# Optimization experiments

Measured on AMD Instinct MI355X. Metric: run time of the kernel, lower is better.

Reference implementation:

```python
import jax, jax.numpy as jnp
import numpy as np

N_NODES = 50000
N_EDGES = 400000
C_IN = 256
HID = 512
C_OUT = 128
N_GRAPHS = 64
BN_EPS = 1e-5


def setup_inputs() -> dict:
    key = jax.random.key(0)
    ks = jax.random.split(key, 18)
    s_in = 1.0 / np.sqrt(C_IN)
    s_h = 1.0 / np.sqrt(HID)
    inp = {
        'x': jax.random.normal(ks[0], (N_NODES, C_IN), jnp.float32),
        'edge_index': jax.random.randint(ks[1], (2, N_EDGES), 0, N_NODES, jnp.int32).astype(jnp.int64),
        'batch': jnp.sort(jax.random.randint(ks[2], (N_NODES,), 0, N_GRAPHS, jnp.int32)).astype(jnp.int64),
        'enc_w': jax.random.normal(ks[3], (C_IN, HID), jnp.float32) * s_in,
        'enc_b': jax.random.normal(ks[4], (HID,), jnp.float32) * s_in,
        'conv_w0': jax.random.normal(ks[5], (2, HID, HID), jnp.float32) * s_h,
        'conv_b0': jax.random.normal(ks[6], (2, HID), jnp.float32) * s_h,
        'bn0_g': jax.random.uniform(ks[7], (2, HID), jnp.float32, 0.5, 1.5),
        'bn0_b': jax.random.normal(ks[8], (2, HID), jnp.float32) * 0.1,
        'conv_w1': jax.random.normal(ks[9], (2, HID, HID), jnp.float32) * s_h,
        'conv_b1': jax.random.normal(ks[10], (2, HID), jnp.float32) * s_h,
        'bn1_g': jax.random.uniform(ks[11], (2, HID), jnp.float32, 0.5, 1.5),
        'bn1_b': jax.random.normal(ks[12], (2, HID), jnp.float32) * 0.1,
        'lin_w': jax.random.normal(ks[13], (HID, HID), jnp.float32) * s_h,
        'lin_b': jax.random.normal(ks[14], (HID,), jnp.float32) * s_h,
        'clf_w': jax.random.normal(ks[15], (HID, C_OUT), jnp.float32) * s_h,
        'clf_b': jax.random.normal(ks[16], (C_OUT,), jnp.float32) * s_h,
    }
    return inp


def _bn_eval(h, gamma, beta):
    # BatchNorm1d in eval mode with default buffers: running_mean=0, running_var=1
    return h * (gamma / jnp.sqrt(1.0 + BN_EPS)) + beta


def reference(x, edge_index, batch, enc_w, enc_b, conv_w0, conv_b0, bn0_g, bn0_b,
              conv_w1, conv_b1, bn1_g, bn1_b, lin_w, lin_b, clf_w, clf_b):
    src, dst = edge_index[0], edge_index[1]
    n = x.shape[0]
    # encoder (gbn output is dead code in the original forward; omitted)
    x = x @ enc_w + enc_b  # [N, HID]
    # GIN_Net: 2 GINConv layers, eps=0, sum aggregation, MLP = Lin-BN-ReLU-Lin-BN
    for i in range(2):
        agg = jax.ops.segment_sum(x[src], dst, num_segments=n)  # scatter-add of neighbor feats
        h = x + agg  # (1 + eps) * x + aggr, eps = 0
        h = h @ conv_w0[i] + conv_b0[i]
        h = jax.nn.relu(_bn_eval(h, bn0_g[i], bn0_b[i]))
        h = h @ conv_w1[i] + conv_b1[i]
        h = _bn_eval(h, bn1_g[i], bn1_b[i])
        # inter-layer relu (dropout p=0 / eval -> identity); skipped after last layer
        x = h if i == 1 else jax.nn.relu(h)
    # global mean pooling over graphs
    sums = jax.ops.segment_sum(x, batch, num_segments=N_GRAPHS)  # [G, HID]
    counts = jax.ops.segment_sum(jnp.ones((n,), x.dtype), batch, num_segments=N_GRAPHS)
    pooled = sums / jnp.maximum(counts, 1.0)[:, None]
    g = jax.nn.gelu(pooled @ lin_w + lin_b, approximate=False)
    # dropout(0.5) identity in eval mode
    return g @ clf_w + clf_b  # [G, C_OUT]
```

## Files before the change

### kernel.cpp

```cpp
#include <hip/hip_runtime.h>
#include <hip/hip_bf16.h>
#include <stdint.h>

#define NN 50000
#define M_PAD 50048
#define NE 400000
#define CIN 256
#define KF 320
#define HID 512
#define COUT 128
#define NG 64
#define SCAN_NB ((NN + 255) / 256)
#define MT128 (M_PAD / 128)
#define GEMM_BLOCKS 512

typedef short bf16x8 __attribute__((ext_vector_type(8)));
typedef float f32x4 __attribute__((ext_vector_type(4)));
typedef unsigned int u32x2 __attribute__((ext_vector_type(2)));

__device__ inline float bf2f(unsigned short u) {
    union { unsigned int i; float f; } v; v.i = ((unsigned int)u) << 16; return v.f;
}
__device__ inline unsigned short f2bf(float f) {
    union { float f; unsigned int u; } v; v.f = f;
    unsigned int r = v.u + 0x7fffu + ((v.u >> 16) & 1u);
    return (unsigned short)(r >> 16);
}

__device__ inline void async16(const void* g, void* l) {
    __builtin_amdgcn_global_load_lds((const __attribute__((address_space(1))) void*)g,
                                     (__attribute__((address_space(3))) void*)l, 16, 0, 0);
}


__global__ void k_f32_to_bf16(const float* __restrict__ in, unsigned short* __restrict__ out, int n4) {
    int i = blockIdx.x * blockDim.x + threadIdx.x;
    if (i < n4) {
        float4 v = ((const float4*)in)[i];
        ushort4 o;
        o.x = f2bf(v.x); o.y = f2bf(v.y); o.z = f2bf(v.z); o.w = f2bf(v.w);
        ((ushort4*)out)[i] = o;
    }
}

__global__ void k_transpose_cvt(const float* __restrict__ in, unsigned short* __restrict__ out, int K, int N) {
    __shared__ float tile[32][33];
    int bx = blockIdx.x * 32, by = blockIdx.y * 32;
    int tx = threadIdx.x & 31, ty = threadIdx.x >> 5;
    for (int i = 0; i < 32; i += 8)
        tile[ty + i][tx] = in[(size_t)(by + ty + i) * N + bx + tx];
    __syncthreads();
    for (int i = 0; i < 32; i += 8)
        out[(size_t)(bx + ty + i) * K + by + tx] = f2bf(tile[tx][ty + i]);
}

__global__ void k_fuse_w0(const float* __restrict__ enc_w, const float* __restrict__ enc_b,
                          const float* __restrict__ W0, unsigned short* __restrict__ WfT) {
    int n = blockIdx.x;
    __shared__ float col[HID];
    for (int j = threadIdx.x; j < HID; j += 256) col[j] = W0[(size_t)j * HID + n];
    __syncthreads();
    int k = threadIdx.x;
    float acc = 0.f;
    for (int j = 0; j < HID; j++) acc += enc_w[(size_t)k * HID + j] * col[j];
    WfT[(size_t)n * KF + k] = f2bf(acc);
    if (k == 0) {
        float v = 0.f;
        for (int j = 0; j < HID; j++) v += enc_b[j] * col[j];
        WfT[(size_t)n * KF + 256] = f2bf(v);
    }
    if (k >= 1 && k < 64) WfT[(size_t)n * KF + 256 + k] = 0;
}

__global__ void k_affine(const float* __restrict__ enc_b,
                         const float* __restrict__ cb0, const float* __restrict__ bg0, const float* __restrict__ bb0,
                         const float* __restrict__ cb1, const float* __restrict__ bg1, const float* __restrict__ bb1,
                         float* __restrict__ scale, float* __restrict__ shift) {
    int c = threadIdx.x;
    const float inv = 0.9999950000374997f;
    scale[c] = 1.f; shift[c] = enc_b[c];
    for (int l = 0; l < 2; l++) {
        float s0 = bg0[l * HID + c] * inv;
        scale[(1 + 2 * l) * HID + c] = s0;
        shift[(1 + 2 * l) * HID + c] = cb0[l * HID + c] * s0 + bb0[l * HID + c];
        float s1 = bg1[l * HID + c] * inv;
        scale[(2 + 2 * l) * HID + c] = s1;
        shift[(2 + 2 * l) * HID + c] = cb1[l * HID + c] * s1 + bb1[l * HID + c];
    }
}


__global__ void k_hist(const int* __restrict__ dst, int* __restrict__ indeg, int n) {
    int i = blockIdx.x * blockDim.x + threadIdx.x;
    if (i < n) atomicAdd(&indeg[dst[i]], 1);
}

__global__ void k_scan1(const int* __restrict__ indeg, int* __restrict__ local,
                        int* __restrict__ blocksum, int n) {
    __shared__ int s[256];
    int t = threadIdx.x;
    int i = blockIdx.x * 256 + t;
    int v = (i < n) ? indeg[i] : 0;
    s[t] = v;
    __syncthreads();
    for (int d = 1; d < 256; d <<= 1) {
        int u = (t >= d) ? s[t - d] : 0;
        __syncthreads();
        s[t] += u;
        __syncthreads();
    }
    if (i < n) local[i] = s[t] - v;
    if (t == 255) blocksum[blockIdx.x] = s[255];
}

__global__ void k_scan2(int* __restrict__ blocksum, int nb) {
    __shared__ int s[256];
    int t = threadIdx.x;
    int v = (t < nb) ? blocksum[t] : 0;
    s[t] = v;
    __syncthreads();
    for (int d = 1; d < 256; d <<= 1) {
        int u = (t >= d) ? s[t - d] : 0;
        __syncthreads();
        s[t] += u;
        __syncthreads();
    }
    if (t < nb) blocksum[t] = s[t] - v;
}

__global__ void k_scan3(const int* __restrict__ local, const int* __restrict__ blocksum,
                        const int* __restrict__ indeg, int* __restrict__ off,
                        int* __restrict__ cursor, int n) {
    int i = blockIdx.x * 256 + threadIdx.x;
    if (i < n) {
        int o = local[i] + blocksum[blockIdx.x];
        off[i] = o;
        cursor[i] = o;
        if (i == n - 1) off[n] = o + indeg[i];
    }
}

__global__ void k_fill(const int* __restrict__ src, const int* __restrict__ dst,
                       int* __restrict__ cursor, int* __restrict__ csr, int n) {
    int i = blockIdx.x * blockDim.x + threadIdx.x;
    if (i < n) {
        int p = atomicAdd(&cursor[dst[i]], 1);
        csr[p] = src[i];
    }
}


__global__ void k_aggregate0(const unsigned short* __restrict__ x, const int* __restrict__ off,
                             const int* __restrict__ csr, unsigned short* __restrict__ z) {
    int wid = (int)((blockIdx.x * blockDim.x + threadIdx.x) >> 6);
    if (wid >= NN) return;
    int lane = threadIdx.x & 63;
    const uint2* xr = (const uint2*)x;
    uint2 v = xr[(size_t)wid * 64 + lane];
    float acc[4];
    {
        unsigned short* p = (unsigned short*)&v;
        for (int i = 0; i < 4; i++) acc[i] = bf2f(p[i]);
    }
    int e0 = off[wid], e1 = off[wid + 1];
    int e = e0;
    for (; e + 3 < e1; e += 4) {
        int u0 = csr[e], u1 = csr[e + 1], u2 = csr[e + 2], u3 = csr[e + 3];
        uint2 v0 = xr[(size_t)u0 * 64 + lane];
        uint2 v1 = xr[(size_t)u1 * 64 + lane];
        uint2 v2 = xr[(size_t)u2 * 64 + lane];
        uint2 v3 = xr[(size_t)u3 * 64 + lane];
        unsigned short* p0 = (unsigned short*)&v0;
        unsigned short* p1 = (unsigned short*)&v1;
        unsigned short* p2 = (unsigned short*)&v2;
        unsigned short* p3 = (unsigned short*)&v3;
#pragma unroll
        for (int i = 0; i < 4; i++)
            acc[i] += (bf2f(p0[i]) + bf2f(p1[i])) + (bf2f(p2[i]) + bf2f(p3[i]));
    }
    for (; e < e1; e++) {
        int u = csr[e];
        uint2 vu = xr[(size_t)u * 64 + lane];
        unsigned short* p = (unsigned short*)&vu;
#pragma unroll
        for (int i = 0; i < 4; i++) acc[i] += bf2f(p[i]);
    }
    uint2 o;
    unsigned short* po = (unsigned short*)&o;
    for (int i = 0; i < 4; i++) po[i] = f2bf(acc[i]);
    uint2* zr = (uint2*)z;
    zr[(size_t)wid * 80 + lane] = o;
    if (lane < 16) {
        uint2 ex; ex.x = 0; ex.y = 0;
        if (lane == 0) ex.x = (unsigned)f2bf((float)(1 + e1 - e0));
        zr[(size_t)wid * 80 + 64 + lane] = ex;
    }
}


__global__ void k_aggregate(const unsigned short* __restrict__ x, const int* __restrict__ off,
                            const int* __restrict__ csr, unsigned short* __restrict__ h) {
    int wid = (int)((blockIdx.x * blockDim.x + threadIdx.x) >> 6);
    if (wid >= NN) return;
    int lane = threadIdx.x & 63;
    const uint4* xr = (const uint4*)x;
    uint4 v = xr[(size_t)wid * 64 + lane];
    float acc[8];
    {
        unsigned short* p = (unsigned short*)&v;
        for (int i = 0; i < 8; i++) acc[i] = bf2f(p[i]);
    }
    int e0 = off[wid], e1 = off[wid + 1];
    int e = e0;
    for (; e + 3 < e1; e += 4) {
        int u0 = csr[e], u1 = csr[e + 1], u2 = csr[e + 2], u3 = csr[e + 3];
        uint4 v0 = xr[(size_t)u0 * 64 + lane];
        uint4 v1 = xr[(size_t)u1 * 64 + lane];
        uint4 v2 = xr[(size_t)u2 * 64 + lane];
        uint4 v3 = xr[(size_t)u3 * 64 + lane];
        unsigned short* p0 = (unsigned short*)&v0;
        unsigned short* p1 = (unsigned short*)&v1;
        unsigned short* p2 = (unsigned short*)&v2;
        unsigned short* p3 = (unsigned short*)&v3;
#pragma unroll
        for (int i = 0; i < 8; i++)
            acc[i] += (bf2f(p0[i]) + bf2f(p1[i])) + (bf2f(p2[i]) + bf2f(p3[i]));
    }
    for (; e < e1; e++) {
        int u = csr[e];
        uint4 vu = xr[(size_t)u * 64 + lane];
        unsigned short* p = (unsigned short*)&vu;
#pragma unroll
        for (int i = 0; i < 8; i++) acc[i] += bf2f(p[i]);
    }
    uint4 o;
    unsigned short* po = (unsigned short*)&o;
    for (int i = 0; i < 8; i++) po[i] = f2bf(acc[i]);
    ((uint4*)h)[(size_t)wid * 64 + lane] = o;
}


template <int RELU, int NSTEPS>
__global__ __launch_bounds__(256, 2) void k_gemm(const unsigned short* __restrict__ A,
                                                 const unsigned short* __restrict__ WT,
                                                 const float* __restrict__ scale,
                                                 const float* __restrict__ shift,
                                                 unsigned short* __restrict__ out) {
    constexpr int K = NSTEPS * 64;
    __shared__ char lds[69632];
    const int tid = threadIdx.x, w = tid >> 6, lane = tid & 63;
    const int wr = w >> 1, wc = w & 1;
    const int lr = lane & 15, lh = lane >> 4;

    {
        float2 s2 = *(const float2*)(scale + tid * 2);
        float2 h2 = *(const float2*)(shift + tid * 2);
        *(float2*)(lds + 65536 + tid * 8) = s2;
        *(float2*)(lds + 67584 + tid * 8) = h2;
    }
    __syncthreads();

    const int b = blockIdx.x;
    const int xcd = b & 7, slot = b >> 3;
    const int xs = (xcd < 4) ? xcd * 196 : 784 + (xcd - 4) * 195;
    const int xcnt = (xcd < 4) ? 196 : 195;
    const int ntiles = (xcnt - slot + 63) >> 6;
    int t = xs + slot;

    int ldsoff[4], roff[4];
#pragma unroll
    for (int ci = 0; ci < 4; ci++) {
        int cc = w * 4 + ci;
        ldsoff[ci] = cc * 1024;
        roff[ci] = ((cc >> 1) * 16 + lr) * K + (cc & 1) * 32 + lh * 8;
    }

    const unsigned short* gA[4];
    const unsigned short* gB[4];
    {
        int tile_m = (t >> 2) * 128, n0 = (t & 3) * 128;
#pragma unroll
        for (int ci = 0; ci < 4; ci++) {
            gA[ci] = A + (size_t)tile_m * K + roff[ci];
            gB[ci] = WT + (size_t)n0 * K + roff[ci];
        }
    }

#pragma unroll
    for (int ci = 0; ci < 4; ci++) { async16(gA[ci], lds + ldsoff[ci]); async16(gB[ci], lds + 16384 + ldsoff[ci]); }
#pragma unroll
    for (int ci = 0; ci < 4; ci++) { async16(gA[ci] + 64, lds + 32768 + ldsoff[ci]); async16(gB[ci] + 64, lds + 32768 + 16384 + ldsoff[ci]); }

    for (int i = 0; i < ntiles; i++) {
        const bool last = (i == ntiles - 1);
        const unsigned short* nA[4];
        const unsigned short* nB[4];
        {
            int tn = last ? t : t + 64;
            int tile_m = (tn >> 2) * 128, n0 = (tn & 3) * 128;
#pragma unroll
            for (int ci = 0; ci < 4; ci++) {
                nA[ci] = A + (size_t)tile_m * K + roff[ci];
                nB[ci] = WT + (size_t)n0 * K + roff[ci];
            }
        }

        f32x4 acc[4][4];
#pragma unroll
        for (int x = 0; x < 4; x++)
#pragma unroll
            for (int y = 0; y < 4; y++) acc[x][y] = f32x4{0.f, 0.f, 0.f, 0.f};

#pragma unroll
        for (int ks = 0; ks < NSTEPS; ks++) {
            const int cur = (ks & 1) << 15;
            if (i > 0 && ks < 2)                 asm volatile("s_waitcnt vmcnt(24)" ::: "memory");
            else if (last && ks == NSTEPS - 1)   asm volatile("s_waitcnt vmcnt(0)" ::: "memory");
            else                                 asm volatile("s_waitcnt vmcnt(8)" ::: "memory");
            __builtin_amdgcn_s_barrier();
            __builtin_amdgcn_sched_barrier(0);
#pragma unroll
            for (int kf = 0; kf < 2; kf++) {
                bf16x8 a[4], bb[4];
#pragma unroll
                for (int mf = 0; mf < 4; mf++)
                    a[mf] = *(const bf16x8*)(lds + cur + ((wr * 4 + mf) * 2 + kf) * 1024 + lane * 16);
#pragma unroll
                for (int nf = 0; nf < 4; nf++)
                    bb[nf] = *(const bf16x8*)(lds + cur + 16384 + ((wc * 4 + nf) * 2 + kf) * 1024 + lane * 16);
#pragma unroll
                for (int mf = 0; mf < 4; mf++)
#pragma unroll
                    for (int nf = 0; nf < 4; nf++)
                        acc[mf][nf] = __builtin_amdgcn_mfma_f32_16x16x32_bf16(bb[nf], a[mf], acc[mf][nf], 0, 0, 0);
            }
            __builtin_amdgcn_sched_barrier(0);
            __builtin_amdgcn_s_barrier();
            if (ks + 2 < NSTEPS) {
                int ko = (ks + 2) << 6;
#pragma unroll
                for (int ci = 0; ci < 4; ci++) {
                    async16(gA[ci] + ko, lds + cur + ldsoff[ci]);
                    async16(gB[ci] + ko, lds + cur + 16384 + ldsoff[ci]);
                }
            } else if (!last) {
                int ko = (ks + 2 - NSTEPS) << 6;
#pragma unroll
                for (int ci = 0; ci < 4; ci++) {
                    async16(nA[ci] + ko, lds + cur + ldsoff[ci]);
                    async16(nB[ci] + ko, lds + cur + 16384 + ldsoff[ci]);
                }
            }
        }

        {
            int tile_m = (t >> 2) * 128, n0 = (t & 3) * 128;
#pragma unroll
            for (int nf = 0; nf < 4; nf++) {
                int col = n0 + wc * 64 + nf * 16 + lh * 4;
                f32x4 sc = *(const f32x4*)(lds + 65536 + ((wc * 64 + nf * 16 + lh * 4) << 2) + (n0 << 2));
                f32x4 sh = *(const f32x4*)(lds + 67584 + ((wc * 64 + nf * 16 + lh * 4) << 2) + (n0 << 2));
#pragma unroll
                for (int mf = 0; mf < 4; mf++) {
                    int row = tile_m + wr * 64 + mf * 16 + lr;
                    float y0 = acc[mf][nf][0] * sc[0] + sh[0];
                    float y1 = acc[mf][nf][1] * sc[1] + sh[1];
                    float y2 = acc[mf][nf][2] * sc[2] + sh[2];
                    float y3 = acc[mf][nf][3] * sc[3] + sh[3];
                    if (RELU) {
                        y0 = fmaxf(y0, 0.f); y1 = fmaxf(y1, 0.f);
                        y2 = fmaxf(y2, 0.f); y3 = fmaxf(y3, 0.f);
                    }
                    u32x2 pd;
                    pd[0] = (unsigned)f2bf(y0) | ((unsigned)f2bf(y1) << 16);
                    pd[1] = (unsigned)f2bf(y2) | ((unsigned)f2bf(y3) << 16);
                    unsigned long long ap = (unsigned long long)(out + (size_t)row * HID + col);
                    asm volatile("global_store_dwordx2 %0, %1, off" :: "v"(ap), "v"(pd) : "memory");
                }
            }
        }

        if (!last) {
#pragma unroll
            for (int ci = 0; ci < 4; ci++) { gA[ci] = nA[ci]; gB[ci] = nB[ci]; }
            t += 64;
        }
    }
}


__global__ void k_bounds(const int* __restrict__ batch, int* __restrict__ bounds) {
    int t = threadIdx.x;
    if (t <= NG) {
        int lo = 0, hi = NN;
        while (lo < hi) { int mid = (lo + hi) >> 1; if (batch[mid] < t) lo = mid + 1; else hi = mid; }
        bounds[t] = lo;
    }
}

__global__ void k_pool(const unsigned short* __restrict__ x, const int* __restrict__ bounds,
                       float* __restrict__ pooled) {
    int g = blockIdx.x, s = blockIdx.y, t = threadIdx.x;
    int b0 = bounds[g], b1 = bounds[g + 1];
    int len = b1 - b0;
    int r0 = b0 + (int)((long long)len * s / 8);
    int r1 = b0 + (int)((long long)len * (s + 1) / 8);
    float acc = 0.f;
    for (int r = r0; r < r1; r++) acc += bf2f(x[(size_t)r * HID + t]);
    if (r1 > r0) atomicAdd(&pooled[g * HID + t], acc);
}

__global__ void k_tailgemm(const float* __restrict__ pooledSum, const int* __restrict__ bounds,
                           const float* __restrict__ W1, const float* __restrict__ scale,
                           const float* __restrict__ shift, float* __restrict__ xfp) {
    int g = blockIdx.x, t = threadIdx.x;
    __shared__ float row[HID];
    int cnt = bounds[g + 1] - bounds[g];
    float invc = 1.f / fmaxf((float)cnt, 1.f);
    row[t] = pooledSum[g * HID + t] * invc;
    __syncthreads();
    float acc = 0.f;
    for (int k = 0; k < HID; k++) acc += row[k] * W1[(size_t)k * HID + t];
    xfp[g * HID + t] = acc * scale[t] + shift[t];
}

__global__ void k_head1(const float* __restrict__ xfp, const float* __restrict__ lin_w,
                        const float* __restrict__ lin_b, float* __restrict__ gout) {
    int g = blockIdx.x, t = threadIdx.x;
    __shared__ float row[HID];
    row[t] = xfp[g * HID + t];
    __syncthreads();
    float acc = lin_b[t];
    for (int k = 0; k < HID; k++) acc += row[k] * lin_w[(size_t)k * HID + t];
    gout[g * HID + t] = 0.5f * acc * (1.f + erff(acc * 0.7071067811865475f));
}

__global__ void k_head2(const float* __restrict__ gbuf, const float* __restrict__ clf_w,
                        const float* __restrict__ clf_b, float* __restrict__ out) {
    int g = blockIdx.x, t = threadIdx.x;
    __shared__ float row[HID];
    for (int k = t; k < HID; k += 128) row[k] = gbuf[g * HID + k];
    __syncthreads();
    float acc = clf_b[t];
    for (int k = 0; k < HID; k++) acc += row[k] * clf_w[(size_t)k * COUT + t];
    out[g * COUT + t] = acc;
}


extern "C" void kernel_launch(void* const* d_in, const int* in_sizes, int n_in,
                              void* d_out, int out_size, void* d_ws, size_t ws_size,
                              hipStream_t stream) {
    const float* x_f32   = (const float*)d_in[0];
    const int*   ei      = (const int*)d_in[1];
    const int*   batch   = (const int*)d_in[2];
    const float* enc_w   = (const float*)d_in[3];
    const float* enc_b   = (const float*)d_in[4];
    const float* conv_w0 = (const float*)d_in[5];
    const float* conv_b0 = (const float*)d_in[6];
    const float* bn0_g   = (const float*)d_in[7];
    const float* bn0_b   = (const float*)d_in[8];
    const float* conv_w1 = (const float*)d_in[9];
    const float* conv_b1 = (const float*)d_in[10];
    const float* bn1_g   = (const float*)d_in[11];
    const float* bn1_b   = (const float*)d_in[12];
    const float* lin_w   = (const float*)d_in[13];
    const float* lin_b   = (const float*)d_in[14];
    const float* clf_w   = (const float*)d_in[15];
    const float* clf_b   = (const float*)d_in[16];
    const int* srcp = ei;
    const int* dstp = ei + NE;

    char* ws = (char*)d_ws;
    size_t o = 0;
    auto alloc = [&](size_t b) { size_t r = o; o += (b + 255) & ~(size_t)255; return r; };
    unsigned short* buf0 = (unsigned short*)(ws + alloc((size_t)M_PAD * HID * 2));
    unsigned short* buf1 = (unsigned short*)(ws + alloc((size_t)M_PAD * HID * 2));
    unsigned short* buf2 = (unsigned short*)(ws + alloc((size_t)M_PAD * HID * 2));
    unsigned short* xbf  = buf0;
    unsigned short* zbuf = buf2;
    unsigned short* WfT  = (unsigned short*)(ws + alloc((size_t)HID * KF * 2));
    unsigned short* c0T  = (unsigned short*)(ws + alloc((size_t)HID * HID * 2));
    unsigned short* c1T  = (unsigned short*)(ws + alloc((size_t)HID * HID * 2));
    float* aff_scale = (float*)(ws + alloc(5 * HID * 4));
    float* aff_shift = (float*)(ws + alloc(5 * HID * 4));
    int* indeg  = (int*)(ws + alloc((size_t)NN * 4));
    int* off    = (int*)(ws + alloc((size_t)(NN + 1) * 4));
    int* cursor = (int*)(ws + alloc((size_t)NN * 4));
    int* csr    = (int*)(ws + alloc((size_t)NE * 4));
    int* scan_local = (int*)(ws + alloc((size_t)NN * 4));
    int* scan_bsum  = (int*)(ws + alloc((size_t)256 * 4));
    int* bounds = (int*)(ws + alloc((size_t)(NG + 1) * 4));
    float* pooledSum = (float*)(ws + alloc((size_t)NG * HID * 4));
    float* xfp       = (float*)(ws + alloc((size_t)NG * HID * 4));
    float* gbuf      = (float*)(ws + alloc((size_t)NG * HID * 4));
    (void)ws_size; (void)n_in; (void)in_sizes; (void)out_size;

    hipMemsetAsync(indeg, 0, (size_t)NN * 4, stream);
    hipMemsetAsync(pooledSum, 0, (size_t)NG * HID * 4, stream);

    k_f32_to_bf16<<<(NN * CIN / 4 + 255) / 256, 256, 0, stream>>>(x_f32, xbf, NN * CIN / 4);
    k_fuse_w0<<<HID, 256, 0, stream>>>(enc_w, enc_b, conv_w0, WfT);
    k_transpose_cvt<<<dim3(16, 16), 256, 0, stream>>>(conv_w0 + HID * HID, c0T, HID, HID);
    k_transpose_cvt<<<dim3(16, 16), 256, 0, stream>>>(conv_w1, c1T, HID, HID);
    k_affine<<<1, 512, 0, stream>>>(enc_b, conv_b0, bn0_g, bn0_b, conv_b1, bn1_g, bn1_b,
                                    aff_scale, aff_shift);

    k_hist<<<(NE + 255) / 256, 256, 0, stream>>>(dstp, indeg, NE);
    k_scan1<<<SCAN_NB, 256, 0, stream>>>(indeg, scan_local, scan_bsum, NN);
    k_scan2<<<1, 256, 0, stream>>>(scan_bsum, SCAN_NB);
    k_scan3<<<SCAN_NB, 256, 0, stream>>>(scan_local, scan_bsum, indeg, off, cursor, NN);
    k_fill<<<(NE + 255) / 256, 256, 0, stream>>>(srcp, dstp, cursor, csr, NE);
    k_bounds<<<1, 128, 0, stream>>>(batch, bounds);

    k_aggregate0<<<(NN * 64) / 256, 256, 0, stream>>>(xbf, off, csr, zbuf);
    k_gemm<1, KF / 64><<<GEMM_BLOCKS, 256, 0, stream>>>(zbuf, WfT,
                                                        aff_scale + 1 * HID, aff_shift + 1 * HID, buf0);
    k_gemm<1, HID / 64><<<GEMM_BLOCKS, 256, 0, stream>>>(buf0, c1T,
                                                         aff_scale + 2 * HID, aff_shift + 2 * HID, buf2);

    k_aggregate<<<(NN * 64) / 256, 256, 0, stream>>>(buf2, off, csr, buf1);
    k_gemm<1, HID / 64><<<GEMM_BLOCKS, 256, 0, stream>>>(buf1, c0T,
                                                         aff_scale + 3 * HID, aff_shift + 3 * HID, buf2);

    k_pool<<<dim3(NG, 8), 512, 0, stream>>>(buf2, bounds, pooledSum);
    k_tailgemm<<<NG, 512, 0, stream>>>(pooledSum, bounds, conv_w1 + HID * HID,
                                       aff_scale + 4 * HID, aff_shift + 4 * HID, xfp);
    k_head1<<<NG, 512, 0, stream>>>(xfp, lin_w, lin_b, gbuf);
    k_head2<<<NG, 128, 0, stream>>>(gbuf, clf_w, clf_b, (float*)d_out);
}
```

Baseline: 478.9 us.

## Triple-buffer A tiles and keep per-column scale/shift in registers

The GEMM pipeline now gives the A operand three LDS stages and B two, so A loads are issued three k-steps ahead while B stays two ahead. Each block's column tile is fixed across its persistent loop, which allows scale/shift to be held in registers instead of LDS and the next-tile pointers to be advanced by a constant stride. Raises s_setprio around the MFMA section. The LDS footprint grows to 80KB, which may limit two blocks per CU, and the vmcnt bookkeeping becomes more fragile.

```diff
diff --git a/kernel.cpp b/kernel.cpp
--- a/kernel.cpp
+++ b/kernel.cpp
@@ -247,18 +247,10 @@
                                                  const float* __restrict__ shift,
                                                  unsigned short* __restrict__ out) {
     constexpr int K = NSTEPS * 64;
-    __shared__ char lds[69632];
+    __shared__ char lds[81920];
     const int tid = threadIdx.x, w = tid >> 6, lane = tid & 63;
     const int wr = w >> 1, wc = w & 1;
     const int lr = lane & 15, lh = lane >> 4;
-
-    {
-        float2 s2 = *(const float2*)(scale + tid * 2);
-        float2 h2 = *(const float2*)(shift + tid * 2);
-        *(float2*)(lds + 65536 + tid * 8) = s2;
-        *(float2*)(lds + 67584 + tid * 8) = h2;
-    }
-    __syncthreads();
 
     const int b = blockIdx.x;
     const int xcd = b & 7, slot = b >> 3;
@@ -266,6 +258,16 @@
     const int xcnt = (xcd < 4) ? 196 : 195;
     const int ntiles = (xcnt - slot + 63) >> 6;
     int t = xs + slot;
+    const int n0 = (t & 3) * 128;
+
+    f32x4 rsc[4], rsh[4];
+#pragma unroll
+    for (int nf = 0; nf < 4; nf++) {
+        int col = n0 + wc * 64 + nf * 16 + lh * 4;
+        rsc[nf] = *(const f32x4*)(scale + col);
+        rsh[nf] = *(const f32x4*)(shift + col);
+    }
+    asm volatile("s_waitcnt vmcnt(0)" ::: "memory");
 
     int ldsoff[4], roff[4];
 #pragma unroll
@@ -275,10 +277,11 @@
         roff[ci] = ((cc >> 1) * 16 + lr) * K + (cc & 1) * 32 + lh * 8;
     }
 
+    const int dA = 2048 * K;
     const unsigned short* gA[4];
     const unsigned short* gB[4];
     {
-        int tile_m = (t >> 2) * 128, n0 = (t & 3) * 128;
+        int tile_m = (t >> 2) * 128;
 #pragma unroll
         for (int ci = 0; ci < 4; ci++) {
             gA[ci] = A + (size_t)tile_m * K + roff[ci];
@@ -286,25 +289,22 @@
         }
     }
 
-#pragma unroll
-    for (int ci = 0; ci < 4; ci++) { async16(gA[ci], lds + ldsoff[ci]); async16(gB[ci], lds + 16384 + ldsoff[ci]); }
-#pragma unroll
-    for (int ci = 0; ci < 4; ci++) { async16(gA[ci] + 64, lds + 32768 + ldsoff[ci]); async16(gB[ci] + 64, lds + 32768 + 16384 + ldsoff[ci]); }
+    int aoff[3] = {0, 16384, 32768};
+    int bpar = 0;
+
+#pragma unroll
+    for (int ci = 0; ci < 4; ci++) async16(gA[ci], lds + aoff[0] + ldsoff[ci]);
+#pragma unroll
+    for (int ci = 0; ci < 4; ci++) async16(gB[ci], lds + 49152 + ldsoff[ci]);
+#pragma unroll
+    for (int ci = 0; ci < 4; ci++) async16(gA[ci] + 64, lds + aoff[1] + ldsoff[ci]);
+#pragma unroll
+    for (int ci = 0; ci < 4; ci++) async16(gB[ci] + 64, lds + 49152 + 16384 + ldsoff[ci]);
+#pragma unroll
+    for (int ci = 0; ci < 4; ci++) async16(gA[ci] + 128, lds + aoff[2] + ldsoff[ci]);
 
     for (int i = 0; i < ntiles; i++) {
         const bool last = (i == ntiles - 1);
-        const unsigned short* nA[4];
-        const unsigned short* nB[4];
-        {
-            int tn = last ? t : t + 64;
-            int tile_m = (tn >> 2) * 128, n0 = (tn & 3) * 128;
-#pragma unroll
-            for (int ci = 0; ci < 4; ci++) {
-                nA[ci] = A + (size_t)tile_m * K + roff[ci];
-                nB[ci] = WT + (size_t)n0 * K + roff[ci];
-            }
-        }
-
         f32x4 acc[4][4];
 #pragma unroll
         for (int x = 0; x < 4; x++)
@@ -313,60 +313,69 @@
 
 #pragma unroll
         for (int ks = 0; ks < NSTEPS; ks++) {
-            const int cur = (ks & 1) << 15;
-            if (i > 0 && ks < 2)                 asm volatile("s_waitcnt vmcnt(24)" ::: "memory");
+            const int ao = aoff[ks % 3];
+            const int bo = 49152 + (((ks & 1) ^ bpar) << 14);
+            if (i > 0 && ks < 2)                 asm volatile("s_waitcnt vmcnt(28)" ::: "memory");
+            else if (last && ks == NSTEPS - 2)   asm volatile("s_waitcnt vmcnt(8)" ::: "memory");
             else if (last && ks == NSTEPS - 1)   asm volatile("s_waitcnt vmcnt(0)" ::: "memory");
-            else                                 asm volatile("s_waitcnt vmcnt(8)" ::: "memory");
+            else                                 asm volatile("s_waitcnt vmcnt(12)" ::: "memory");
             __builtin_amdgcn_s_barrier();
             __builtin_amdgcn_sched_barrier(0);
+            __builtin_amdgcn_s_setprio(1);
 #pragma unroll
             for (int kf = 0; kf < 2; kf++) {
                 bf16x8 a[4], bb[4];
 #pragma unroll
                 for (int mf = 0; mf < 4; mf++)
-                    a[mf] = *(const bf16x8*)(lds + cur + ((wr * 4 + mf) * 2 + kf) * 1024 + lane * 16);
+                    a[mf] = *(const bf16x8*)(lds + ao + ((wr * 4 + mf) * 2 + kf) * 1024 + lane * 16);
 #pragma unroll
                 for (int nf = 0; nf < 4; nf++)
-                    bb[nf] = *(const bf16x8*)(lds + cur + 16384 + ((wc * 4 + nf) * 2 + kf) * 1024 + lane * 16);
+                    bb[nf] = *(const bf16x8*)(lds + bo + ((wc * 4 + nf) * 2 + kf) * 1024 + lane * 16);
 #pragma unroll
                 for (int mf = 0; mf < 4; mf++)
 #pragma unroll
                     for (int nf = 0; nf < 4; nf++)
                         acc[mf][nf] = __builtin_amdgcn_mfma_f32_16x16x32_bf16(bb[nf], a[mf], acc[mf][nf], 0, 0, 0);
             }
+            __builtin_amdgcn_s_setprio(0);
             __builtin_amdgcn_sched_barrier(0);
             __builtin_amdgcn_s_barrier();
+            {
+                constexpr int BT = 1;
+                (void)BT;
+            }
             if (ks + 2 < NSTEPS) {
                 int ko = (ks + 2) << 6;
 #pragma unroll
-                for (int ci = 0; ci < 4; ci++) {
-                    async16(gA[ci] + ko, lds + cur + ldsoff[ci]);
-                    async16(gB[ci] + ko, lds + cur + 16384 + ldsoff[ci]);
-                }
+                for (int ci = 0; ci < 4; ci++) async16(gB[ci] + ko, lds + bo + ldsoff[ci]);
             } else if (!last) {
                 int ko = (ks + 2 - NSTEPS) << 6;
 #pragma unroll
-                for (int ci = 0; ci < 4; ci++) {
-                    async16(nA[ci] + ko, lds + cur + ldsoff[ci]);
-                    async16(nB[ci] + ko, lds + cur + 16384 + ldsoff[ci]);
-                }
+                for (int ci = 0; ci < 4; ci++) async16(gB[ci] + ko, lds + bo + ldsoff[ci]);
+            }
+            if (ks + 3 < NSTEPS) {
+                int ko = (ks + 3) << 6;
+#pragma unroll
+                for (int ci = 0; ci < 4; ci++) async16(gA[ci] + ko, lds + ao + ldsoff[ci]);
+            } else if (!last) {
+                int ko = (ks + 3 - NSTEPS) << 6;
+#pragma unroll
+                for (int ci = 0; ci < 4; ci++) async16(gA[ci] + dA + ko, lds + ao + ldsoff[ci]);
             }
         }
 
         {
-            int tile_m = (t >> 2) * 128, n0 = (t & 3) * 128;
+            int tile_m = (t >> 2) * 128;
 #pragma unroll
             for (int nf = 0; nf < 4; nf++) {
                 int col = n0 + wc * 64 + nf * 16 + lh * 4;
-                f32x4 sc = *(const f32x4*)(lds + 65536 + ((wc * 64 + nf * 16 + lh * 4) << 2) + (n0 << 2));
-                f32x4 sh = *(const f32x4*)(lds + 67584 + ((wc * 64 + nf * 16 + lh * 4) << 2) + (n0 << 2));
 #pragma unroll
                 for (int mf = 0; mf < 4; mf++) {
                     int row = tile_m + wr * 64 + mf * 16 + lr;
-                    float y0 = acc[mf][nf][0] * sc[0] + sh[0];
-                    float y1 = acc[mf][nf][1] * sc[1] + sh[1];
-                    float y2 = acc[mf][nf][2] * sc[2] + sh[2];
-                    float y3 = acc[mf][nf][3] * sc[3] + sh[3];
+                    float y0 = acc[mf][nf][0] * rsc[nf][0] + rsh[nf][0];
+                    float y1 = acc[mf][nf][1] * rsc[nf][1] + rsh[nf][1];
+                    float y2 = acc[mf][nf][2] * rsc[nf][2] + rsh[nf][2];
+                    float y3 = acc[mf][nf][3] * rsc[nf][3] + rsh[nf][3];
                     if (RELU) {
                         y0 = fmaxf(y0, 0.f); y1 = fmaxf(y1, 0.f);
                         y2 = fmaxf(y2, 0.f); y3 = fmaxf(y3, 0.f);
@@ -382,8 +391,15 @@
 
         if (!last) {
 #pragma unroll
-            for (int ci = 0; ci < 4; ci++) { gA[ci] = nA[ci]; gB[ci] = nB[ci]; }
+            for (int ci = 0; ci < 4; ci++) gA[ci] += dA;
             t += 64;
+            constexpr int R = NSTEPS % 3;
+            if (R != 0) {
+                int a0 = aoff[0], a1 = aoff[1], a2 = aoff[2];
+                if (R == 2) { aoff[0] = a2; aoff[1] = a0; aoff[2] = a1; }
+                else        { aoff[0] = a1; aoff[1] = a2; aoff[2] = a0; }
+            }
+            bpar ^= (NSTEPS & 1);
         }
     }
 }
```

Result: no change. 484.7 us (+1.2%).

## Switch GEMM to one-shot 256x256 tiles with 512-thread workgroups

Applied to the files above, without the earlier changes.

Replaces the persistent 128x128-tile GEMM, which looped over tiles and prefetched the next tile, with a non-persistent kernel. Each 512-thread workgroup now computes one 256x256 output tile, and tiles are assigned with an XCD-aware block remap. M padding grows to a multiple of 256 and scale/shift are read straight from global memory instead of staged in LDS. The larger tile raises operand reuse per LDS load. In exchange, the 128KB LDS buffer likely limits each CU to one workgroup, 392 workgroups leave a ragged final wave, and the next tile is no longer prefetched.

```diff
diff --git a/kernel.cpp b/kernel.cpp
--- a/kernel.cpp
+++ b/kernel.cpp
@@ -3,7 +3,7 @@
 #include <stdint.h>
 
 #define NN 50000
-#define M_PAD 50048
+#define M_PAD 50176
 #define NE 400000
 #define CIN 256
 #define KF 320
@@ -11,12 +11,10 @@
 #define COUT 128
 #define NG 64
 #define SCAN_NB ((NN + 255) / 256)
-#define MT128 (M_PAD / 128)
-#define GEMM_BLOCKS 512
+#define GEMM_NWG 392
 
 typedef short bf16x8 __attribute__((ext_vector_type(8)));
 typedef float f32x4 __attribute__((ext_vector_type(4)));
-typedef unsigned int u32x2 __attribute__((ext_vector_type(2)));
 
 __device__ inline float bf2f(unsigned short u) {
     union { unsigned int i; float f; } v; v.i = ((unsigned int)u) << 16; return v.f;
@@ -241,149 +239,101 @@
 
 
 template <int RELU, int NSTEPS>
-__global__ __launch_bounds__(256, 2) void k_gemm(const unsigned short* __restrict__ A,
+__global__ __launch_bounds__(512, 2) void k_gemm(const unsigned short* __restrict__ A,
                                                  const unsigned short* __restrict__ WT,
                                                  const float* __restrict__ scale,
                                                  const float* __restrict__ shift,
                                                  unsigned short* __restrict__ out) {
     constexpr int K = NSTEPS * 64;
-    __shared__ char lds[69632];
+    __shared__ char lds[131072];
     const int tid = threadIdx.x, w = tid >> 6, lane = tid & 63;
-    const int wr = w >> 1, wc = w & 1;
+    const int wr = w >> 2, wc = w & 3;
     const int lr = lane & 15, lh = lane >> 4;
 
-    {
-        float2 s2 = *(const float2*)(scale + tid * 2);
-        float2 h2 = *(const float2*)(shift + tid * 2);
-        *(float2*)(lds + 65536 + tid * 8) = s2;
-        *(float2*)(lds + 67584 + tid * 8) = h2;
-    }
-    __syncthreads();
-
-    const int b = blockIdx.x;
-    const int xcd = b & 7, slot = b >> 3;
-    const int xs = (xcd < 4) ? xcd * 196 : 784 + (xcd - 4) * 195;
-    const int xcnt = (xcd < 4) ? 196 : 195;
-    const int ntiles = (xcnt - slot + 63) >> 6;
-    int t = xs + slot;
-
-    int ldsoff[4], roff[4];
-#pragma unroll
-    for (int ci = 0; ci < 4; ci++) {
-        int cc = w * 4 + ci;
-        ldsoff[ci] = cc * 1024;
-        roff[ci] = ((cc >> 1) * 16 + lr) * K + (cc & 1) * 32 + lh * 8;
-    }
+    int orig = blockIdx.x;
+    int wgid = (orig & 7) * 49 + (orig >> 3);
+    int tile_m = (wgid >> 1) * 256;
+    int n0 = (wgid & 1) * 256;
 
     const unsigned short* gA[4];
     const unsigned short* gB[4];
-    {
-        int tile_m = (t >> 2) * 128, n0 = (t & 3) * 128;
-#pragma unroll
-        for (int ci = 0; ci < 4; ci++) {
-            gA[ci] = A + (size_t)tile_m * K + roff[ci];
-            gB[ci] = WT + (size_t)n0 * K + roff[ci];
+    int ldsoff[4];
+#pragma unroll
+    for (int ci = 0; ci < 4; ci++) {
+        int c = w * 4 + ci;
+        int f = c >> 1, kf = c & 1;
+        ldsoff[ci] = c * 1024;
+        gA[ci] = A + (size_t)(tile_m + f * 16 + lr) * K + kf * 32 + lh * 8;
+        gB[ci] = WT + (size_t)(n0 + f * 16 + lr) * K + kf * 32 + lh * 8;
+    }
+
+    f32x4 acc[8][4];
+#pragma unroll
+    for (int x = 0; x < 8; x++)
+#pragma unroll
+        for (int y = 0; y < 4; y++) acc[x][y] = f32x4{0.f, 0.f, 0.f, 0.f};
+
+#pragma unroll
+    for (int ci = 0; ci < 4; ci++) async16(gA[ci], lds + ldsoff[ci]);
+#pragma unroll
+    for (int ci = 0; ci < 4; ci++) async16(gB[ci], lds + 32768 + ldsoff[ci]);
+#pragma unroll
+    for (int ci = 0; ci < 4; ci++) async16(gA[ci] + 64, lds + 65536 + ldsoff[ci]);
+#pragma unroll
+    for (int ci = 0; ci < 4; ci++) async16(gB[ci] + 64, lds + 65536 + 32768 + ldsoff[ci]);
+
+#pragma unroll
+    for (int ks = 0; ks < NSTEPS; ks++) {
+        const int cur = (ks & 1) << 16;
+        if (ks < NSTEPS - 1) asm volatile("s_waitcnt vmcnt(8)" ::: "memory");
+        else                 asm volatile("s_waitcnt vmcnt(0)" ::: "memory");
+        __builtin_amdgcn_s_barrier();
+        __builtin_amdgcn_sched_barrier(0);
+#pragma unroll
+        for (int kf = 0; kf < 2; kf++) {
+            bf16x8 a[8], bb[4];
+#pragma unroll
+            for (int mf = 0; mf < 8; mf++)
+                a[mf] = *(const bf16x8*)(lds + cur + ((wr * 8 + mf) * 2 + kf) * 1024 + lane * 16);
+#pragma unroll
+            for (int nf = 0; nf < 4; nf++)
+                bb[nf] = *(const bf16x8*)(lds + cur + 32768 + ((wc * 4 + nf) * 2 + kf) * 1024 + lane * 16);
+#pragma unroll
+            for (int mf = 0; mf < 8; mf++)
+#pragma unroll
+                for (int nf = 0; nf < 4; nf++)
+                    acc[mf][nf] = __builtin_amdgcn_mfma_f32_16x16x32_bf16(bb[nf], a[mf], acc[mf][nf], 0, 0, 0);
         }
-    }
-
-#pragma unroll
-    for (int ci = 0; ci < 4; ci++) { async16(gA[ci], lds + ldsoff[ci]); async16(gB[ci], lds + 16384 + ldsoff[ci]); }
-#pragma unroll
-    for (int ci = 0; ci < 4; ci++) { async16(gA[ci] + 64, lds + 32768 + ldsoff[ci]); async16(gB[ci] + 64, lds + 32768 + 16384 + ldsoff[ci]); }
-
-    for (int i = 0; i < ntiles; i++) {
-        const bool last = (i == ntiles - 1);
-        const unsigned short* nA[4];
-        const unsigned short* nB[4];
-        {
-            int tn = last ? t : t + 64;
-            int tile_m = (tn >> 2) * 128, n0 = (tn & 3) * 128;
-#pragma unroll
-            for (int ci = 0; ci < 4; ci++) {
-                nA[ci] = A + (size_t)tile_m * K + roff[ci];
-                nB[ci] = WT + (size_t)n0 * K + roff[ci];
+        __builtin_amdgcn_sched_barrier(0);
+        __builtin_amdgcn_s_barrier();
+        if (ks + 2 < NSTEPS) {
+            int ko = (ks + 2) << 6;
+#pragma unroll
+            for (int ci = 0; ci < 4; ci++) async16(gA[ci] + ko, lds + cur + ldsoff[ci]);
+#pragma unroll
+            for (int ci = 0; ci < 4; ci++) async16(gB[ci] + ko, lds + cur + 32768 + ldsoff[ci]);
+        }
+    }
+
+#pragma unroll
+    for (int nf = 0; nf < 4; nf++) {
+        int col = n0 + wc * 64 + nf * 16 + lh * 4;
+        float4 sc = *(const float4*)&scale[col];
+        float4 sh = *(const float4*)&shift[col];
+#pragma unroll
+        for (int mf = 0; mf < 8; mf++) {
+            int row = tile_m + wr * 128 + mf * 16 + lr;
+            float y0 = acc[mf][nf][0] * sc.x + sh.x;
+            float y1 = acc[mf][nf][1] * sc.y + sh.y;
+            float y2 = acc[mf][nf][2] * sc.z + sh.z;
+            float y3 = acc[mf][nf][3] * sc.w + sh.w;
+            if (RELU) {
+                y0 = fmaxf(y0, 0.f); y1 = fmaxf(y1, 0.f);
+                y2 = fmaxf(y2, 0.f); y3 = fmaxf(y3, 0.f);
             }
-        }
-
-        f32x4 acc[4][4];
-#pragma unroll
-        for (int x = 0; x < 4; x++)
-#pragma unroll
-            for (int y = 0; y < 4; y++) acc[x][y] = f32x4{0.f, 0.f, 0.f, 0.f};
-
-#pragma unroll
-        for (int ks = 0; ks < NSTEPS; ks++) {
-            const int cur = (ks & 1) << 15;
-            if (i > 0 && ks < 2)                 asm volatile("s_waitcnt vmcnt(24)" ::: "memory");
-            else if (last && ks == NSTEPS - 1)   asm volatile("s_waitcnt vmcnt(0)" ::: "memory");
-            else                                 asm volatile("s_waitcnt vmcnt(8)" ::: "memory");
-            __builtin_amdgcn_s_barrier();
-            __builtin_amdgcn_sched_barrier(0);
-#pragma unroll
-            for (int kf = 0; kf < 2; kf++) {
-                bf16x8 a[4], bb[4];
-#pragma unroll
-                for (int mf = 0; mf < 4; mf++)
-                    a[mf] = *(const bf16x8*)(lds + cur + ((wr * 4 + mf) * 2 + kf) * 1024 + lane * 16);
-#pragma unroll
-                for (int nf = 0; nf < 4; nf++)
-                    bb[nf] = *(const bf16x8*)(lds + cur + 16384 + ((wc * 4 + nf) * 2 + kf) * 1024 + lane * 16);
-#pragma unroll
-                for (int mf = 0; mf < 4; mf++)
-#pragma unroll
-                    for (int nf = 0; nf < 4; nf++)
-                        acc[mf][nf] = __builtin_amdgcn_mfma_f32_16x16x32_bf16(bb[nf], a[mf], acc[mf][nf], 0, 0, 0);
-            }
-            __builtin_amdgcn_sched_barrier(0);
-            __builtin_amdgcn_s_barrier();
-            if (ks + 2 < NSTEPS) {
-                int ko = (ks + 2) << 6;
-#pragma unroll
-                for (int ci = 0; ci < 4; ci++) {
-                    async16(gA[ci] + ko, lds + cur + ldsoff[ci]);
-                    async16(gB[ci] + ko, lds + cur + 16384 + ldsoff[ci]);
-                }
-            } else if (!last) {
-                int ko = (ks + 2 - NSTEPS) << 6;
-#pragma unroll
-                for (int ci = 0; ci < 4; ci++) {
-                    async16(nA[ci] + ko, lds + cur + ldsoff[ci]);
-                    async16(nB[ci] + ko, lds + cur + 16384 + ldsoff[ci]);
-                }
-            }
-        }
-
-        {
-            int tile_m = (t >> 2) * 128, n0 = (t & 3) * 128;
-#pragma unroll
-            for (int nf = 0; nf < 4; nf++) {
-                int col = n0 + wc * 64 + nf * 16 + lh * 4;
-                f32x4 sc = *(const f32x4*)(lds + 65536 + ((wc * 64 + nf * 16 + lh * 4) << 2) + (n0 << 2));
-                f32x4 sh = *(const f32x4*)(lds + 67584 + ((wc * 64 + nf * 16 + lh * 4) << 2) + (n0 << 2));
-#pragma unroll
-                for (int mf = 0; mf < 4; mf++) {
-                    int row = tile_m + wr * 64 + mf * 16 + lr;
-                    float y0 = acc[mf][nf][0] * sc[0] + sh[0];
-                    float y1 = acc[mf][nf][1] * sc[1] + sh[1];
-                    float y2 = acc[mf][nf][2] * sc[2] + sh[2];
-                    float y3 = acc[mf][nf][3] * sc[3] + sh[3];
-                    if (RELU) {
-                        y0 = fmaxf(y0, 0.f); y1 = fmaxf(y1, 0.f);
-                        y2 = fmaxf(y2, 0.f); y3 = fmaxf(y3, 0.f);
-                    }
-                    u32x2 pd;
-                    pd[0] = (unsigned)f2bf(y0) | ((unsigned)f2bf(y1) << 16);
-                    pd[1] = (unsigned)f2bf(y2) | ((unsigned)f2bf(y3) << 16);
-                    unsigned long long ap = (unsigned long long)(out + (size_t)row * HID + col);
-                    asm volatile("global_store_dwordx2 %0, %1, off" :: "v"(ap), "v"(pd) : "memory");
-                }
-            }
-        }
-
-        if (!last) {
-#pragma unroll
-            for (int ci = 0; ci < 4; ci++) { gA[ci] = nA[ci]; gB[ci] = nB[ci]; }
-            t += 64;
+            ushort4 pk;
+            pk.x = f2bf(y0); pk.y = f2bf(y1); pk.z = f2bf(y2); pk.w = f2bf(y3);
+            *(ushort4*)(out + (size_t)row * HID + col) = pk;
         }
     }
 }
@@ -513,14 +463,14 @@
     k_bounds<<<1, 128, 0, stream>>>(batch, bounds);
 
     k_aggregate0<<<(NN * 64) / 256, 256, 0, stream>>>(xbf, off, csr, zbuf);
-    k_gemm<1, KF / 64><<<GEMM_BLOCKS, 256, 0, stream>>>(zbuf, WfT,
-                                                        aff_scale + 1 * HID, aff_shift + 1 * HID, buf0);
-    k_gemm<1, HID / 64><<<GEMM_BLOCKS, 256, 0, stream>>>(buf0, c1T,
-                                                         aff_scale + 2 * HID, aff_shift + 2 * HID, buf2);
+    k_gemm<1, KF / 64><<<GEMM_NWG, 512, 0, stream>>>(zbuf, WfT,
+                                                     aff_scale + 1 * HID, aff_shift + 1 * HID, buf0);
+    k_gemm<1, HID / 64><<<GEMM_NWG, 512, 0, stream>>>(buf0, c1T,
+                                                      aff_scale + 2 * HID, aff_shift + 2 * HID, buf2);
 
     k_aggregate<<<(NN * 64) / 256, 256, 0, stream>>>(buf2, off, csr, buf1);
-    k_gemm<1, HID / 64><<<GEMM_BLOCKS, 256, 0, stream>>>(buf1, c0T,
-                                                         aff_scale + 3 * HID, aff_shift + 3 * HID, buf2);
+    k_gemm<1, HID / 64><<<GEMM_NWG, 512, 0, stream>>>(buf1, c0T,
+                                                      aff_scale + 3 * HID, aff_shift + 3 * HID, buf2);
 
     k_pool<<<dim3(NG, 8), 512, 0, stream>>>(buf2, bounds, pooledSum);
     k_tailgemm<<<NG, 512, 0, stream>>>(pooledSum, bounds, conv_w1 + HID * HID,
```

After: 453.5 us. 5.3% less time.
